# Kernel tuning notes

Measured on AMD Instinct MI355X. Metric: run time of the kernel, lower is better.

The kernel has to match this reference:

```python
import jax, jax.numpy as jnp
import numpy as np

N_HEAD = 16
MASKED_BIAS = -10000.0


def setup_inputs() -> dict:
    key = jax.random.key(0)
    k1, k2, k3 = jax.random.split(key, 3)
    B, T, E = 2, 2048, 1024
    return {
        "stacked": jax.random.normal(k1, (B, T, E), dtype=jnp.float32),
        "w_attn": jax.random.normal(k2, (E, 3 * E), dtype=jnp.float32) * 0.02,
        "b_attn": jnp.zeros((3 * E,), dtype=jnp.float32),
        "w_proj": jax.random.normal(k3, (E, E), dtype=jnp.float32) * 0.02,
        "b_proj": jnp.zeros((E,), dtype=jnp.float32),
    }


def reference(stacked, w_attn, b_attn, w_proj, b_proj):
    B, T, E = stacked.shape
    nh = N_HEAD
    dh = E // nh
    # Conv1D (GPT-2): x @ W + b
    qkv = stacked @ w_attn + b_attn            # (B, T, 3E)
    q, k, v = jnp.split(qkv, 3, axis=-1)
    q = q.reshape(B, T, nh, dh).transpose(0, 2, 1, 3)  # (B, nh, T, dh)
    k = k.reshape(B, T, nh, dh).transpose(0, 2, 1, 3)
    v = v.reshape(B, T, nh, dh).transpose(0, 2, 1, 3)
    # scores = Q @ K^T / sqrt(dh)
    w = jnp.einsum("bhtd,bhsd->bhts", q, k) / jnp.sqrt(jnp.float32(dh))
    causal = jnp.tril(jnp.ones((T, T), dtype=bool))
    w = jnp.where(causal, w, jnp.float32(MASKED_BIAS))
    w = jax.nn.softmax(w, axis=-1)
    out = jnp.einsum("bhts,bhsd->bhtd", w, v)  # (B, nh, T, dh)
    out = out.transpose(0, 2, 1, 3).reshape(B, T, E)
    attn_z = out @ w_proj + b_proj
    return attn_z
```

## Files before the change

kernel.cpp:

```cpp
#include <hip/hip_runtime.h>
#include <hip/hip_bf16.h>

#define B_ 2
#define T_ 2048
#define E_ 1024
#define NH 16
#define M_ (B_*T_)
#define N3E 3072

typedef __attribute__((ext_vector_type(8))) short short8;
typedef __attribute__((ext_vector_type(4))) float f32x4;

__device__ __forceinline__ unsigned short f2bf(float f) {
  unsigned u = __builtin_bit_cast(unsigned, f);
  unsigned r = 0x7FFFu + ((u >> 16) & 1u);
  return (unsigned short)((u + r) >> 16);
}

__device__ __forceinline__ float bf2f(unsigned short s) {
  return __builtin_bit_cast(float, ((unsigned)s) << 16);
}

__device__ __forceinline__ unsigned cvtpk(float a, float b) {
  unsigned r;
  asm("v_cvt_pk_bf16_f32 %0, %1, %2" : "=v"(r) : "v"(a), "v"(b));
  return r;
}

__device__ __forceinline__ float exp2fast(float x) {
  float r;
  asm("v_exp_f32 %0, %1" : "=v"(r) : "v"(x));
  return r;
}

__device__ __forceinline__ void gload16(const void* g, void* l) {
  __builtin_amdgcn_global_load_lds(
      (const __attribute__((address_space(1))) unsigned int*)g,
      (__attribute__((address_space(3))) unsigned int*)l, 16, 0, 0);
}

__global__ __launch_bounds__(256) void prep_kernel(
    const float* __restrict__ stacked, const float* __restrict__ w_attn,
    const float* __restrict__ w_proj, unsigned short* __restrict__ Abf,
    unsigned short* __restrict__ WaT, unsigned short* __restrict__ WpT) {
  __shared__ float tile[32][33];
  const int bx = blockIdx.x;
  const int tid = threadIdx.x;
  if (bx < 2048) {
    int i = bx * 256 + tid;
    const float4* p = (const float4*)stacked + (size_t)i * 2;
    float4 a = p[0], b = p[1];
    short8 o;
    o[0] = (short)f2bf(a.x); o[1] = (short)f2bf(a.y);
    o[2] = (short)f2bf(a.z); o[3] = (short)f2bf(a.w);
    o[4] = (short)f2bf(b.x); o[5] = (short)f2bf(b.y);
    o[6] = (short)f2bf(b.z); o[7] = (short)f2bf(b.w);
    *(short8*)(Abf + (size_t)i * 8) = o;
    return;
  }
  const float* in;
  unsigned short* out;
  int R, C, c0, r0;
  if (bx < 5120) {
    int b = bx - 2048;
    in = w_attn; out = WaT; R = E_; C = N3E;
    c0 = (b % 96) * 32; r0 = (b / 96) * 32;
  } else {
    int b = bx - 5120;
    in = w_proj; out = WpT; R = E_; C = E_;
    c0 = (b % 32) * 32; r0 = (b / 32) * 32;
  }
  int tx = tid & 31, ty = tid >> 5;
#pragma unroll
  for (int i = 0; i < 4; i++) {
    int r = ty + i * 8;
    tile[r][tx] = in[(size_t)(r0 + r) * C + c0 + tx];
  }
  __syncthreads();
#pragma unroll
  for (int i = 0; i < 4; i++) {
    int r = ty + i * 8;
    out[(size_t)(c0 + r) * R + r0 + tx] = f2bf(tile[tx][r]);
  }
}

__global__ __launch_bounds__(256) void vtrans_kernel(
    const unsigned short* __restrict__ qkv, unsigned short* __restrict__ Vt) {
  const int s0 = blockIdx.x * 64;
  const int c0 = blockIdx.y * 64;
  const int b = blockIdx.z;
  __shared__ unsigned short t[64][72];
  const int tid = threadIdx.x;
  const size_t rs = 3 * E_;
  const unsigned short* src = qkv + (size_t)(b * T_) * rs + 2 * E_;
#pragma unroll
  for (int p = 0; p < 2; p++) {
    int idx = tid + p * 256;
    int r = idx >> 3, c = (idx & 7) * 8;
    *(short8*)&t[r][c] = *(const short8*)(src + (size_t)(s0 + r) * rs + c0 + c);
  }
  __syncthreads();
#pragma unroll
  for (int p = 0; p < 2; p++) {
    int idx = tid + p * 256;
    int dr = idx >> 3, sc = (idx & 7) * 8;
    short8 o;
#pragma unroll
    for (int j = 0; j < 8; j++) o[j] = (short)t[sc + j][dr];
    *(short8*)&Vt[(size_t)(b * E_ + c0 + dr) * T_ + s0 + sc] = o;
  }
}

template <int OUTF32>
__global__ __launch_bounds__(256) void gemm_bt(
    const unsigned short* __restrict__ A, const unsigned short* __restrict__ Bt,
    const float* __restrict__ bias, void* __restrict__ outp,
    int M, int N, int K) {
  __shared__ __attribute__((aligned(16))) unsigned short Asm[2][128 * 32];
  __shared__ __attribute__((aligned(16))) unsigned short Bsm[2][128 * 32];
  const int tid = threadIdx.x;
  const int lane = tid & 63;
  const int wid = tid >> 6;
  const int wr = wid >> 1, wc = wid & 1;
  const int li = lane & 15, g = lane >> 4;

  const int ntx = N >> 7;
  const int nwg = (M >> 7) * ntx;
  const int cpx = nwg >> 3;
  const int logical = (blockIdx.x & 7) * cpx + (blockIdx.x >> 3);
  const int bm = (logical / ntx) << 7;
  const int bn = (logical % ntx) << 7;

  f32x4 acc[4][4] = {};

  const int srow = tid >> 2;
  const int scol = (tid & 3) * 8;
  const unsigned short* Ag = A + (size_t)(bm + srow) * K + scol;
  const unsigned short* Bg = Bt + (size_t)(bn + srow) * K + scol;
  const int ldsoff = tid * 16;

  gload16(Ag, (char*)&Asm[0][0] + ldsoff);
  gload16(Ag + (size_t)64 * K, (char*)&Asm[0][0] + ldsoff + 4096);
  gload16(Bg, (char*)&Bsm[0][0] + ldsoff);
  gload16(Bg + (size_t)64 * K, (char*)&Bsm[0][0] + ldsoff + 4096);
  asm volatile("s_waitcnt vmcnt(0)" ::: "memory");
  __syncthreads();

  int cur = 0;
  for (int k0 = 0; k0 < K; k0 += 32) {
    const bool pre = (k0 + 32 < K);
    if (pre) {
      const int k1 = k0 + 32;
      gload16(Ag + k1, (char*)&Asm[cur ^ 1][0] + ldsoff);
      gload16(Ag + (size_t)64 * K + k1,
              (char*)&Asm[cur ^ 1][0] + ldsoff + 4096);
      gload16(Bg + k1, (char*)&Bsm[cur ^ 1][0] + ldsoff);
      gload16(Bg + (size_t)64 * K + k1,
              (char*)&Bsm[cur ^ 1][0] + ldsoff + 4096);
    }
    short8 af[4], bf[4];
#pragma unroll
    for (int i = 0; i < 4; i++)
      af[i] = *(const short8*)&Asm[cur][(wr * 64 + i * 16 + li) * 32 + g * 8];
#pragma unroll
    for (int j = 0; j < 4; j++)
      bf[j] = *(const short8*)&Bsm[cur][(wc * 64 + j * 16 + li) * 32 + g * 8];
    __builtin_amdgcn_s_setprio(1);
#pragma unroll
    for (int i = 0; i < 4; i++)
#pragma unroll
      for (int j = 0; j < 4; j++)
        acc[i][j] = __builtin_amdgcn_mfma_f32_16x16x32_bf16(af[i], bf[j],
                                                            acc[i][j], 0, 0, 0);
    __builtin_amdgcn_s_setprio(0);
    if (pre) asm volatile("s_waitcnt vmcnt(0)" ::: "memory");
    __syncthreads();
    cur ^= 1;
  }

#pragma unroll
  for (int j = 0; j < 4; j++) {
    int col = bn + wc * 64 + j * 16 + li;
    float bs = bias[col];
#pragma unroll
    for (int i = 0; i < 4; i++) {
      int row0 = bm + wr * 64 + i * 16 + g * 4;
#pragma unroll
      for (int r = 0; r < 4; r++) {
        float v = acc[i][j][r] + bs;
        if (OUTF32)
          ((float*)outp)[(size_t)(row0 + r) * N + col] = v;
        else
          ((unsigned short*)outp)[(size_t)(row0 + r) * N + col] = f2bf(v);
      }
    }
  }
}

__device__ __forceinline__ f32x4 mfma16(short8 a, short8 b, f32x4 c) {
  return __builtin_amdgcn_mfma_f32_16x16x32_bf16(a, b, c, 0, 0, 0);
}

__device__ __forceinline__ void attn_tile(
    const unsigned short* Ksm, const unsigned short* Vts,
    unsigned short (*PsmW)[64], short8 qf0, short8 qf1,
    float& m2, float& l2, f32x4* O, int qrel, bool diag, int li, int g) {
  f32x4 S[4];
  __builtin_amdgcn_s_setprio(1);
#pragma unroll
  for (int ct = 0; ct < 4; ct++) {
    int r = ct * 16 + li;
    int sw = r & 7;
    short8 k0f = *(const short8*)&Ksm[r * 64 + ((g ^ sw) << 3)];
    short8 k1f = *(const short8*)&Ksm[r * 64 + (((g + 4) ^ sw) << 3)];
    f32x4 z = {0.f, 0.f, 0.f, 0.f};
    z = mfma16(k0f, qf0, z);
    z = mfma16(k1f, qf1, z);
    S[ct] = z;
  }
  __builtin_amdgcn_s_setprio(0);

  if (diag) {
#pragma unroll
    for (int ct = 0; ct < 4; ct++)
#pragma unroll
      for (int r = 0; r < 4; r++)
        if (ct * 16 + g * 4 + r > qrel) S[ct][r] = -30000.f;
  }

  float tmax = S[0][0];
#pragma unroll
  for (int ct = 0; ct < 4; ct++)
#pragma unroll
    for (int r = 0; r < 4; r++) tmax = fmaxf(tmax, S[ct][r]);
  tmax = fmaxf(tmax, __shfl_xor(tmax, 16));
  tmax = fmaxf(tmax, __shfl_xor(tmax, 32));

  if (__any(tmax > m2 + 11.5f)) {
    float mn = fmaxf(m2, tmax);
    float cs = exp2fast(m2 - mn);
    l2 *= cs;
#pragma unroll
    for (int c2 = 0; c2 < 4; c2++)
#pragma unroll
      for (int r = 0; r < 4; r++) O[c2][r] *= cs;
    m2 = mn;
  }

  float rsum = 0.f;
#pragma unroll
  for (int ct = 0; ct < 4; ct++) {
    float p0 = exp2fast(S[ct][0] - m2);
    float p1 = exp2fast(S[ct][1] - m2);
    float p2 = exp2fast(S[ct][2] - m2);
    float p3 = exp2fast(S[ct][3] - m2);
    rsum += (p0 + p1) + (p2 + p3);
    uint2 pk;
    pk.x = cvtpk(p0, p1);
    pk.y = cvtpk(p2, p3);
    int pc = (2 * ct + (g >> 1)) ^ (li & 7);
    *(uint2*)&PsmW[li][pc * 8 + (g & 1) * 4] = pk;
  }
  rsum += __shfl_xor(rsum, 16);
  rsum += __shfl_xor(rsum, 32);
  l2 += rsum;

  __builtin_amdgcn_s_setprio(1);
#pragma unroll
  for (int kk = 0; kk < 2; kk++) {
    short8 pf = *(const short8*)&PsmW[li][((4 * kk + g) ^ (li & 7)) * 8];
#pragma unroll
    for (int c2 = 0; c2 < 4; c2++) {
      int d = c2 * 16 + li;
      short8 vf = *(const short8*)&Vts[d * 64 + (((kk * 4 + g) ^ (li & 7)) << 3)];
      O[c2] = mfma16(vf, pf, O[c2]);
    }
  }
  __builtin_amdgcn_s_setprio(0);
}

__global__ __launch_bounds__(256) void attn_kernel(
    const unsigned short* __restrict__ qkv, const unsigned short* __restrict__ Vt,
    unsigned short* __restrict__ aout) {
  const int pair = blockIdx.x;
  const int h = blockIdx.y, b = blockIdx.z;
  const int qa = pair, qb = (T_ / 64 - 1) - pair;
  const int tid = threadIdx.x, lane = tid & 63, w = tid >> 6;
  const int li = lane & 15, g = lane >> 4;

  __shared__ __attribute__((aligned(16))) unsigned short Ksm[2][64 * 64];
  __shared__ __attribute__((aligned(16))) unsigned short Vts[2][64 * 64];
  __shared__ __attribute__((aligned(16))) unsigned short Psm[4][16][64];

  const size_t rs = 3 * E_;
  const unsigned short* base = qkv + (size_t)b * T_ * rs + h * 64;
  const unsigned short* Kg = base + E_;
  const unsigned short* Vtg = Vt + (size_t)(b * E_ + h * 64) * T_;

  const float QSC = 0.18033688f;
  short8 qfa0, qfa1, qfb0, qfb1;
  {
    const unsigned short* qrow = base + (size_t)(qa * 64 + w * 16 + li) * rs;
    short8 v0 = *(const short8*)(qrow + g * 8);
    short8 v1 = *(const short8*)(qrow + 32 + g * 8);
    qrow = base + (size_t)(qb * 64 + w * 16 + li) * rs;
    short8 v2 = *(const short8*)(qrow + g * 8);
    short8 v3 = *(const short8*)(qrow + 32 + g * 8);
#pragma unroll
    for (int j = 0; j < 8; j++) {
      qfa0[j] = (short)f2bf(bf2f((unsigned short)v0[j]) * QSC);
      qfa1[j] = (short)f2bf(bf2f((unsigned short)v1[j]) * QSC);
      qfb0[j] = (short)f2bf(bf2f((unsigned short)v2[j]) * QSC);
      qfb1[j] = (short)f2bf(bf2f((unsigned short)v3[j]) * QSC);
    }
  }

  float ma = -1e30f, la = 0.f, mb = -1e30f, lb = 0.f;
  f32x4 Oa[4] = {}, Ob[4] = {};

#pragma unroll
  for (int p = 0; p < 2; p++) {
    int idx = tid + p * 256;
    int r = idx >> 3, ch = idx & 7;
    int sc = (ch ^ (r & 7)) * 8;
    gload16(Kg + (size_t)r * rs + sc, (char*)&Ksm[0][0] + idx * 16);
    gload16(Vtg + (size_t)r * T_ + sc, (char*)&Vts[0][0] + idx * 16);
  }
  asm volatile("s_waitcnt vmcnt(0)" ::: "memory");
  __syncthreads();

  const int nt = qb + 1;
  for (int kv = 0; kv < nt; kv++) {
    const int cur = kv & 1, nxt = cur ^ 1;
    const bool pre = (kv + 1 < nt);
    if (pre) {
      const int s1 = (kv + 1) * 64;
#pragma unroll
      for (int p = 0; p < 2; p++) {
        int idx = tid + p * 256;
        int r = idx >> 3, ch = idx & 7;
        int sc = (ch ^ (r & 7)) * 8;
        gload16(Kg + (size_t)(s1 + r) * rs + sc,
                (char*)&Ksm[nxt][0] + idx * 16);
        gload16(Vtg + (size_t)r * T_ + s1 + sc,
                (char*)&Vts[nxt][0] + idx * 16);
      }
    }

    attn_tile(&Ksm[cur][0], &Vts[cur][0], Psm[w], qfb0, qfb1, mb, lb, Ob,
              qb * 64 + w * 16 + li - kv * 64, kv == qb, li, g);
    if (kv <= qa)
      attn_tile(&Ksm[cur][0], &Vts[cur][0], Psm[w], qfa0, qfa1, ma, la, Oa,
                qa * 64 + w * 16 + li - kv * 64, kv == qa, li, g);

    asm volatile("s_waitcnt vmcnt(0)" ::: "memory");
    __syncthreads();
  }

  const float inva = 1.f / la, invb = 1.f / lb;
  const int rowa = b * T_ + qa * 64 + w * 16 + li;
  const int rowb = b * T_ + qb * 64 + w * 16 + li;
#pragma unroll
  for (int c2 = 0; c2 < 4; c2++) {
    uint2 oa, ob;
    oa.x = cvtpk(Oa[c2][0] * inva, Oa[c2][1] * inva);
    oa.y = cvtpk(Oa[c2][2] * inva, Oa[c2][3] * inva);
    ob.x = cvtpk(Ob[c2][0] * invb, Ob[c2][1] * invb);
    ob.y = cvtpk(Ob[c2][2] * invb, Ob[c2][3] * invb);
    *(uint2*)&aout[(size_t)rowa * E_ + h * 64 + c2 * 16 + g * 4] = oa;
    *(uint2*)&aout[(size_t)rowb * E_ + h * 64 + c2 * 16 + g * 4] = ob;
  }
}

extern "C" void kernel_launch(void* const* d_in, const int* in_sizes, int n_in,
                              void* d_out, int out_size, void* d_ws,
                              size_t ws_size, hipStream_t stream) {
  const float* stacked = (const float*)d_in[0];
  const float* w_attn = (const float*)d_in[1];
  const float* b_attn = (const float*)d_in[2];
  const float* w_proj = (const float*)d_in[3];
  const float* b_proj = (const float*)d_in[4];
  float* out = (float*)d_out;

  unsigned short* Abf = (unsigned short*)d_ws;
  unsigned short* WaT = Abf + (size_t)M_ * E_;
  unsigned short* WpT = WaT + (size_t)N3E * E_;
  unsigned short* qkv = WpT + (size_t)E_ * E_;
  unsigned short* aout = qkv + (size_t)M_ * N3E;
  unsigned short* Vt = aout + (size_t)M_ * E_;

  prep_kernel<<<6144, 256, 0, stream>>>(stacked, w_attn, w_proj, Abf, WaT, WpT);
  gemm_bt<0><<<(M_ / 128) * (N3E / 128), 256, 0, stream>>>(Abf, WaT, b_attn,
                                                           qkv, M_, N3E, E_);
  vtrans_kernel<<<dim3(T_ / 64, E_ / 64, B_), 256, 0, stream>>>(qkv, Vt);
  attn_kernel<<<dim3(T_ / 128, NH, B_), 256, 0, stream>>>(qkv, Vt, aout);
  gemm_bt<1><<<(M_ / 128) * (E_ / 128), 256, 0, stream>>>(aout, WpT, b_proj,
                                                          out, M_, E_, E_);
}
```

Before: 120.5 us.

## Split attention KV range across two blocks per query pair and combine partials

Each causal query-tile pair is now handled by two blocks, each covering half of the key/value range (split-K flash attention). The blocks write unnormalized fp32 partial outputs plus running max and sum to workspace, and a new combine kernel merges them with log-sum-exp rescaling into the bf16 attention output. This doubles the attention grid from 512 to 1024 blocks to improve CU occupancy and per-block latency. In exchange it adds an extra kernel launch and fp32 partial traffic through global memory.

```diff
diff --git a/kernel.cpp b/kernel.cpp
--- a/kernel.cpp
+++ b/kernel.cpp
@@ -281,10 +281,14 @@
 
 __global__ __launch_bounds__(256) void attn_kernel(
     const unsigned short* __restrict__ qkv, const unsigned short* __restrict__ Vt,
-    unsigned short* __restrict__ aout) {
-  const int pair = blockIdx.x;
+    unsigned short* __restrict__ aout, float* __restrict__ Opart,
+    float2* __restrict__ mlbuf) {
+  const int s = blockIdx.x & 1, p = blockIdx.x >> 1;
   const int h = blockIdx.y, b = blockIdx.z;
-  const int qa = pair, qb = (T_ / 64 - 1) - pair;
+  const int qa = p, qb = 31 - p, h0 = 15 - p;
+  const int kv_lo = s ? h0 : 0;
+  const int kv_hi = s ? (qb + 1) : (p + 1 > h0 ? p + 1 : h0);
+  const int qbhi = s ? (qb + 1) : h0;
   const int tid = threadIdx.x, lane = tid & 63, w = tid >> 6;
   const int li = lane & 15, g = lane >> 4;
 
@@ -319,25 +323,26 @@
   f32x4 Oa[4] = {}, Ob[4] = {};
 
 #pragma unroll
-  for (int p = 0; p < 2; p++) {
-    int idx = tid + p * 256;
+  for (int pp = 0; pp < 2; pp++) {
+    int idx = tid + pp * 256;
     int r = idx >> 3, ch = idx & 7;
     int sc = (ch ^ (r & 7)) * 8;
-    gload16(Kg + (size_t)r * rs + sc, (char*)&Ksm[0][0] + idx * 16);
-    gload16(Vtg + (size_t)r * T_ + sc, (char*)&Vts[0][0] + idx * 16);
+    gload16(Kg + (size_t)(kv_lo * 64 + r) * rs + sc,
+            (char*)&Ksm[0][0] + idx * 16);
+    gload16(Vtg + (size_t)r * T_ + kv_lo * 64 + sc,
+            (char*)&Vts[0][0] + idx * 16);
   }
   asm volatile("s_waitcnt vmcnt(0)" ::: "memory");
   __syncthreads();
 
-  const int nt = qb + 1;
-  for (int kv = 0; kv < nt; kv++) {
-    const int cur = kv & 1, nxt = cur ^ 1;
-    const bool pre = (kv + 1 < nt);
+  for (int kv = kv_lo; kv < kv_hi; kv++) {
+    const int cur = (kv - kv_lo) & 1, nxt = cur ^ 1;
+    const bool pre = (kv + 1 < kv_hi);
     if (pre) {
       const int s1 = (kv + 1) * 64;
 #pragma unroll
-      for (int p = 0; p < 2; p++) {
-        int idx = tid + p * 256;
+      for (int pp = 0; pp < 2; pp++) {
+        int idx = tid + pp * 256;
         int r = idx >> 3, ch = idx & 7;
         int sc = (ch ^ (r & 7)) * 8;
         gload16(Kg + (size_t)(s1 + r) * rs + sc,
@@ -347,9 +352,10 @@
       }
     }
 
-    attn_tile(&Ksm[cur][0], &Vts[cur][0], Psm[w], qfb0, qfb1, mb, lb, Ob,
-              qb * 64 + w * 16 + li - kv * 64, kv == qb, li, g);
-    if (kv <= qa)
+    if (kv < qbhi)
+      attn_tile(&Ksm[cur][0], &Vts[cur][0], Psm[w], qfb0, qfb1, mb, lb, Ob,
+                qb * 64 + w * 16 + li - kv * 64, kv == qb, li, g);
+    if (s == 0 && kv <= qa)
       attn_tile(&Ksm[cur][0], &Vts[cur][0], Psm[w], qfa0, qfa1, ma, la, Oa,
                 qa * 64 + w * 16 + li - kv * 64, kv == qa, li, g);
 
@@ -357,19 +363,61 @@
     __syncthreads();
   }
 
-  const float inva = 1.f / la, invb = 1.f / lb;
-  const int rowa = b * T_ + qa * 64 + w * 16 + li;
-  const int rowb = b * T_ + qb * 64 + w * 16 + li;
-#pragma unroll
-  for (int c2 = 0; c2 < 4; c2++) {
-    uint2 oa, ob;
-    oa.x = cvtpk(Oa[c2][0] * inva, Oa[c2][1] * inva);
-    oa.y = cvtpk(Oa[c2][2] * inva, Oa[c2][3] * inva);
-    ob.x = cvtpk(Ob[c2][0] * invb, Ob[c2][1] * invb);
-    ob.y = cvtpk(Ob[c2][2] * invb, Ob[c2][3] * invb);
-    *(uint2*)&aout[(size_t)rowa * E_ + h * 64 + c2 * 16 + g * 4] = oa;
-    *(uint2*)&aout[(size_t)rowb * E_ + h * 64 + c2 * 16 + g * 4] = ob;
-  }
+  {
+    const int pr = p * 64 + w * 16 + li;
+    float* opb = Opart + (((size_t)(s * B_ + b) * NH + h) * 1024 + pr) * 64;
+#pragma unroll
+    for (int c2 = 0; c2 < 4; c2++)
+      *(f32x4*)(opb + c2 * 16 + g * 4) = Ob[c2];
+    if (g == 0)
+      mlbuf[((size_t)(s * B_ + b) * NH + h) * 1024 + pr] =
+          make_float2(mb, lb);
+  }
+  if (s == 0) {
+    const float inva = 1.f / la;
+    const int rowa = b * T_ + qa * 64 + w * 16 + li;
+#pragma unroll
+    for (int c2 = 0; c2 < 4; c2++) {
+      uint2 oa;
+      oa.x = cvtpk(Oa[c2][0] * inva, Oa[c2][1] * inva);
+      oa.y = cvtpk(Oa[c2][2] * inva, Oa[c2][3] * inva);
+      *(uint2*)&aout[(size_t)rowa * E_ + h * 64 + c2 * 16 + g * 4] = oa;
+    }
+  }
+}
+
+__global__ __launch_bounds__(256) void combine_kernel(
+    const float* __restrict__ Opart, const float2* __restrict__ mlbuf,
+    unsigned short* __restrict__ aout) {
+  const int idx = blockIdx.x * 256 + threadIdx.x;
+  const int row = idx >> 3, c8 = (idx & 7) * 8;
+  const int b = row >> 14;
+  const int h = (row >> 10) & 15;
+  const int pr = row & 1023;
+  const int p = pr >> 6, r = pr & 63;
+  const size_t i0 = ((size_t)(0 * B_ + b) * NH + h) * 1024 + pr;
+  const size_t i1 = ((size_t)(1 * B_ + b) * NH + h) * 1024 + pr;
+  float2 ml0 = mlbuf[i0];
+  float2 ml1 = mlbuf[i1];
+  float m = fmaxf(ml0.x, ml1.x);
+  float w0 = exp2fast(ml0.x - m), w1 = exp2fast(ml1.x - m);
+  float inv = 1.f / (ml0.y * w0 + ml1.y * w1);
+  const f32x4* o0 = (const f32x4*)(Opart + i0 * 64 + c8);
+  const f32x4* o1 = (const f32x4*)(Opart + i1 * 64 + c8);
+  f32x4 a0 = o0[0], a1 = o0[1], b0 = o1[0], b1 = o1[1];
+  float v[8];
+#pragma unroll
+  for (int j = 0; j < 4; j++) {
+    v[j] = (a0[j] * w0 + b0[j] * w1) * inv;
+    v[4 + j] = (a1[j] * w0 + b1[j] * w1) * inv;
+  }
+  uint2 lo, hi;
+  lo.x = cvtpk(v[0], v[1]); lo.y = cvtpk(v[2], v[3]);
+  hi.x = cvtpk(v[4], v[5]); hi.y = cvtpk(v[6], v[7]);
+  unsigned short* dst =
+      aout + (size_t)(b * T_ + (31 - p) * 64 + r) * E_ + h * 64 + c8;
+  *(uint2*)dst = lo;
+  *(uint2*)(dst + 4) = hi;
 }
 
 extern "C" void kernel_launch(void* const* d_in, const int* in_sizes, int n_in,
@@ -388,12 +436,16 @@
   unsigned short* qkv = WpT + (size_t)E_ * E_;
   unsigned short* aout = qkv + (size_t)M_ * N3E;
   unsigned short* Vt = aout + (size_t)M_ * E_;
+  float* Opart = (float*)(Vt + (size_t)M_ * E_);
+  float2* mlbuf = (float2*)(Opart + (size_t)2 * B_ * NH * 1024 * 64);
 
   prep_kernel<<<6144, 256, 0, stream>>>(stacked, w_attn, w_proj, Abf, WaT, WpT);
   gemm_bt<0><<<(M_ / 128) * (N3E / 128), 256, 0, stream>>>(Abf, WaT, b_attn,
                                                            qkv, M_, N3E, E_);
   vtrans_kernel<<<dim3(T_ / 64, E_ / 64, B_), 256, 0, stream>>>(qkv, Vt);
-  attn_kernel<<<dim3(T_ / 128, NH, B_), 256, 0, stream>>>(qkv, Vt, aout);
+  attn_kernel<<<dim3(32, NH, B_), 256, 0, stream>>>(qkv, Vt, aout, Opart,
+                                                    mlbuf);
+  combine_kernel<<<1024, 256, 0, stream>>>(Opart, mlbuf, aout);
   gemm_bt<1><<<(M_ / 128) * (E_ / 128), 256, 0, stream>>>(aout, WpT, b_proj,
                                                           out, M_, E_, E_);
 }
```

New measurement: 128.4 us. +6.6%, slower.

## Use 256x256-tile, 512-thread GEMM with staged prefetch for QKV projection

Applied to the files above, without the earlier changes.

Adds a gemm256 kernel for the QKV projection. It uses 256x256 output tiles, 8 waves, a K-step of 64 and double-buffered LDS with XOR swizzle. Prefetches of the next A and B tiles are interleaved with MFMA sub-steps, and priority hints are set around the MFMA blocks. Larger tiles are meant to raise arithmetic intensity and cut global traffic per FLOP. In exchange the launch has only 192 workgroups on 256 CUs, and each block needs 128KB of LDS.

```diff
diff --git a/kernel.cpp b/kernel.cpp
--- a/kernel.cpp
+++ b/kernel.cpp
@@ -37,6 +37,10 @@
   __builtin_amdgcn_global_load_lds(
       (const __attribute__((address_space(1))) unsigned int*)g,
       (__attribute__((address_space(3))) unsigned int*)l, 16, 0, 0);
+}
+
+__device__ __forceinline__ f32x4 mfma16(short8 a, short8 b, f32x4 c) {
+  return __builtin_amdgcn_mfma_f32_16x16x32_bf16(a, b, c, 0, 0, 0);
 }
 
 __global__ __launch_bounds__(256) void prep_kernel(
@@ -111,6 +115,117 @@
   }
 }
 
+__global__ __launch_bounds__(512, 2) void gemm256(
+    const unsigned short* __restrict__ A, const unsigned short* __restrict__ Bt,
+    const float* __restrict__ bias, unsigned short* __restrict__ outp,
+    int M, int N, int K) {
+  __shared__ __attribute__((aligned(16))) unsigned short Asm[2][256 * 64];
+  __shared__ __attribute__((aligned(16))) unsigned short Bsm[2][256 * 64];
+  const int tid = threadIdx.x;
+  const int lane = tid & 63, wid = tid >> 6;
+  const int wr = wid >> 2, wcn = wid & 3;
+  const int li = lane & 15, g = lane >> 4;
+  const int sw = li & 7;
+
+  const int ntx = N >> 8;
+  const int nwg = (M >> 8) * ntx;
+  const int cpx = nwg >> 3;
+  const int logical = (blockIdx.x & 7) * cpx + (blockIdx.x >> 3);
+  const int bm = (logical / ntx) << 8;
+  const int bn = (logical % ntx) << 8;
+
+  f32x4 acc[8][4] = {};
+
+#pragma unroll
+  for (int p = 0; p < 4; p++) {
+    int idx = tid + p * 512;
+    int r = idx >> 3, ch = idx & 7;
+    gload16(A + (size_t)(bm + r) * K + ((ch ^ (r & 7)) << 3),
+            (char*)&Asm[0][0] + idx * 16);
+  }
+#pragma unroll
+  for (int p = 0; p < 4; p++) {
+    int idx = tid + p * 512;
+    int r = idx >> 3, ch = idx & 7;
+    gload16(Bt + (size_t)(bn + r) * K + ((ch ^ (r & 7)) << 3),
+            (char*)&Bsm[0][0] + idx * 16);
+  }
+  asm volatile("s_waitcnt vmcnt(0)" ::: "memory");
+  __syncthreads();
+
+  const int NT = K >> 6;
+  for (int t = 0; t < NT; t++) {
+    const int buf = t & 1;
+    const unsigned short* As = &Asm[buf][0];
+    const unsigned short* Bs = &Bsm[buf][0];
+    const int kn = (t + 1) << 6;
+    const bool pre = (t + 1 < NT);
+#pragma unroll
+    for (int q = 0; q < 4; q++) {
+      const int mh = q >> 1, nh2 = q & 1;
+      short8 a[4][2], bfr[2][2];
+#pragma unroll
+      for (int mf = 0; mf < 4; mf++) {
+        const int R = wr * 128 + (mh * 4 + mf) * 16 + li;
+        a[mf][0] = *(const short8*)&As[R * 64 + ((g ^ sw) << 3)];
+        a[mf][1] = *(const short8*)&As[R * 64 + (((4 + g) ^ sw) << 3)];
+      }
+#pragma unroll
+      for (int nf = 0; nf < 2; nf++) {
+        const int S = wcn * 64 + (nh2 * 2 + nf) * 16 + li;
+        bfr[nf][0] = *(const short8*)&Bs[S * 64 + ((g ^ sw) << 3)];
+        bfr[nf][1] = *(const short8*)&Bs[S * 64 + (((4 + g) ^ sw) << 3)];
+      }
+      if (pre && q == 0) {
+#pragma unroll
+        for (int p = 0; p < 4; p++) {
+          int idx = tid + p * 512;
+          int r = idx >> 3, ch = idx & 7;
+          gload16(A + (size_t)(bm + r) * K + kn + ((ch ^ (r & 7)) << 3),
+                  (char*)&Asm[buf ^ 1][0] + idx * 16);
+        }
+      }
+      if (pre && q == 1) {
+#pragma unroll
+        for (int p = 0; p < 4; p++) {
+          int idx = tid + p * 512;
+          int r = idx >> 3, ch = idx & 7;
+          gload16(Bt + (size_t)(bn + r) * K + kn + ((ch ^ (r & 7)) << 3),
+                  (char*)&Bsm[buf ^ 1][0] + idx * 16);
+        }
+      }
+      __builtin_amdgcn_sched_barrier(0);
+      __builtin_amdgcn_s_setprio(1);
+#pragma unroll
+      for (int mf = 0; mf < 4; mf++)
+#pragma unroll
+        for (int nf = 0; nf < 2; nf++) {
+          f32x4 c = acc[mh * 4 + mf][nh2 * 2 + nf];
+          c = mfma16(a[mf][0], bfr[nf][0], c);
+          c = mfma16(a[mf][1], bfr[nf][1], c);
+          acc[mh * 4 + mf][nh2 * 2 + nf] = c;
+        }
+      __builtin_amdgcn_s_setprio(0);
+      __builtin_amdgcn_sched_barrier(0);
+    }
+    asm volatile("s_waitcnt vmcnt(0)" ::: "memory");
+    __syncthreads();
+  }
+
+#pragma unroll
+  for (int nf = 0; nf < 4; nf++) {
+    int col = bn + wcn * 64 + nf * 16 + li;
+    float bs = bias[col];
+#pragma unroll
+    for (int mf = 0; mf < 8; mf++) {
+      int row0 = bm + wr * 128 + mf * 16 + g * 4;
+#pragma unroll
+      for (int r = 0; r < 4; r++)
+        outp[(size_t)(row0 + r) * N + col] = f2bf(acc[mf][nf][r] + bs);
+    }
+  }
+}
+
 template <int OUTF32>
 __global__ __launch_bounds__(256) void gemm_bt(
     const unsigned short* __restrict__ A, const unsigned short* __restrict__ Bt,
@@ -197,10 +312,6 @@
   }
 }
 
-__device__ __forceinline__ f32x4 mfma16(short8 a, short8 b, f32x4 c) {
-  return __builtin_amdgcn_mfma_f32_16x16x32_bf16(a, b, c, 0, 0, 0);
-}
-
 __device__ __forceinline__ void attn_tile(
     const unsigned short* Ksm, const unsigned short* Vts,
     unsigned short (*PsmW)[64], short8 qf0, short8 qf1,
@@ -390,8 +501,8 @@
   unsigned short* Vt = aout + (size_t)M_ * E_;
 
   prep_kernel<<<6144, 256, 0, stream>>>(stacked, w_attn, w_proj, Abf, WaT, WpT);
-  gemm_bt<0><<<(M_ / 128) * (N3E / 128), 256, 0, stream>>>(Abf, WaT, b_attn,
-                                                           qkv, M_, N3E, E_);
+  gemm256<<<(M_ / 256) * (N3E / 256), 512, 0, stream>>>(Abf, WaT, b_attn, qkv,
+                                                        M_, N3E, E_);
   vtrans_kernel<<<dim3(T_ / 64, E_ / 64, B_), 256, 0, stream>>>(qkv, Vt);
   attn_kernel<<<dim3(T_ / 128, NH, B_), 256, 0, stream>>>(qkv, Vt, aout);
   gemm_bt<1><<<(M_ / 128) * (E_ / 128), 256, 0, stream>>>(aout, WpT, b_proj,
```

Measured after the change: 118.1 us. About the same (-1.9%).
